# Kernel tuning notes

Hardware: AMD Instinct MI355X
Metric: run time of the kernel (lower is better)

## Reference

```python
import jax, jax.numpy as jnp
import numpy as np

K_TOP = 2  # top-k experts per token (MoE k)


def setup_inputs() -> dict:
    key = jax.random.key(0)
    ks = jax.random.split(key, 4)
    B, D, H, E = 4096, 1024, 2048, 8
    x = jax.random.normal(ks[0], (B, D), dtype=jnp.float32)
    w_gate = jax.random.normal(ks[1], (D, E), dtype=jnp.float32) * 0.02
    W1 = jax.random.normal(ks[2], (E, D, H), dtype=jnp.float32) * (1.0 / np.sqrt(D))
    b1 = jnp.zeros((E, H), dtype=jnp.float32)
    W2 = jax.random.normal(ks[3], (E, H, D), dtype=jnp.float32) * (1.0 / np.sqrt(H))
    b2 = jnp.zeros((E, D), dtype=jnp.float32)
    return {"x": x, "w_gate": w_gate, "W1": W1, "b1": b1, "W2": W2, "b2": b2}


def _top_k_gates(logits, k):
    # noisy_top_k_gating, eval path (noisy_gating=False / train=False):
    # softmax over the top-k logits, scattered back to [B, E]; other gates are 0.
    B, E = logits.shape
    top_logits, top_idx = jax.lax.top_k(logits, k)       # [B, k]
    top_gates = jax.nn.softmax(top_logits, axis=-1)      # [B, k]
    rows = jnp.arange(B)[:, None]
    gates = jnp.zeros((B, E), dtype=logits.dtype).at[rows, top_idx].set(top_gates)
    return gates


def reference(x, w_gate, W1, b1, W2, b2):
    # Gating
    logits = x @ w_gate                                  # [B, E]
    gates = _top_k_gates(logits, K_TOP)                  # [B, E], sparse (top-k nonzero)
    # Experts: MLP(fc1 -> relu -> fc2) per expert. Dense-all-experts form is
    # mathematically identical to dispatch/combine since zero gates contribute 0.
    h = jax.nn.relu(jnp.einsum('bd,edh->beh', x, W1) + b1[None])   # [B, E, H]
    y = jnp.einsum('beh,ehd->bed', h, W2) + b2[None]               # [B, E, D]
    out = jnp.einsum('be,bed->bd', gates, y)                       # gated scatter-combine
    return out
```

## Files before the change

kernel.cpp:

```cpp
#include <hip/hip_runtime.h>

#define B_TOK 4096
#define DDIM  1024
#define HDIM  2048
#define NEXP  8
#define MAXTOK 4096
#define BM 128
#define BN 128
#define BK 64

#define OFF_W1T  0ull
#define OFF_W2T  33554432ull
#define OFF_XB   67108864ull
#define OFF_H    75497472ull
#define OFF_Y    109051904ull
#define OFF_TOK  125829120ull
#define OFF_GATE 125960192ull
#define OFF_PAIR 126091264ull
#define OFF_CNT  126124032ull
#define OFF_OFFS 126124096ull
#define OFF_EIDX (OFF_Y)
#define OFF_GCO  (OFF_Y + 16384ull)

typedef __attribute__((ext_vector_type(4))) float f32x4;
typedef __attribute__((ext_vector_type(8))) short bf16x8;

static __device__ __forceinline__ unsigned short f2bf(float f) {
    unsigned u = __builtin_bit_cast(unsigned, f);
    unsigned r = (u + 0x7FFFu + ((u >> 16) & 1u)) >> 16;
    return (unsigned short)r;
}
static __device__ __forceinline__ float bf2f(unsigned short s) {
    unsigned u = ((unsigned)s) << 16;
    return __builtin_bit_cast(float, u);
}

#define AS1(p) ((const __attribute__((address_space(1))) void*)(p))
#define AS3(p) ((__attribute__((address_space(3))) void*)(p))

__global__ void __launch_bounds__(256) gating_logits_kernel(
    const float* __restrict__ x, const float* __restrict__ wg,
    int* __restrict__ eidx, float* __restrict__ gco, short* __restrict__ Xb) {
    int wave = threadIdx.x >> 6;
    int lane = threadIdx.x & 63;
    int b = blockIdx.x * 4 + wave;
    float acc[NEXP];
#pragma unroll
    for (int e = 0; e < NEXP; e++) acc[e] = 0.f;
    const float* xr = x + (size_t)b * DDIM;
    short* xbr = Xb + (size_t)b * DDIM;
#pragma unroll
    for (int i = 0; i < DDIM / 64; i++) {
        int d = i * 64 + lane;
        float xv = xr[d];
        xbr[d] = (short)f2bf(xv);
        const float4* wrow = (const float4*)(wg + (size_t)d * NEXP);
        float4 w0 = wrow[0], w1 = wrow[1];
        acc[0] += xv * w0.x; acc[1] += xv * w0.y; acc[2] += xv * w0.z; acc[3] += xv * w0.w;
        acc[4] += xv * w1.x; acc[5] += xv * w1.y; acc[6] += xv * w1.z; acc[7] += xv * w1.w;
    }
#pragma unroll
    for (int off = 32; off >= 1; off >>= 1)
#pragma unroll
        for (int e = 0; e < NEXP; e++) acc[e] += __shfl_xor(acc[e], off);
    if (lane == 0) {
        int i1 = 0; float m1 = acc[0];
        for (int e = 1; e < NEXP; e++) if (acc[e] > m1) { m1 = acc[e]; i1 = e; }
        int i2 = (i1 == 0) ? 1 : 0; float m2 = -1e30f;
        for (int e = 0; e < NEXP; e++) { if (e == i1) continue; if (acc[e] > m2) { m2 = acc[e]; i2 = e; } }
        float g1 = 1.f / (1.f + expf(m2 - m1));
        eidx[b] = i1 | (i2 << 16);
        gco[b] = g1;
    }
}

__global__ void __launch_bounds__(256) build_kernel(
    const int* __restrict__ eidx, const float* __restrict__ gco,
    int* __restrict__ counts, int* __restrict__ tok,
    float* __restrict__ gate, int* __restrict__ pair) {
    __shared__ int lhist[NEXP];
    __shared__ int gbase[NEXP];
    int t = threadIdx.x;
    if (t < NEXP) lhist[t] = 0;
    __syncthreads();
    int b = blockIdx.x * 256 + t;
    int ep = eidx[b];
    int e1 = ep & 0xffff, e2 = ep >> 16;
    float g1 = gco[b], g2 = 1.f - g1;
    int l1 = atomicAdd(&lhist[e1], 1);
    int l2 = atomicAdd(&lhist[e2], 1);
    __syncthreads();
    if (t < NEXP) gbase[t] = atomicAdd(&counts[t], lhist[t]);
    __syncthreads();
    int s1 = gbase[e1] + l1, s2 = gbase[e2] + l2;
    tok[e1 * MAXTOK + s1] = b; gate[e1 * MAXTOK + s1] = g1; pair[b * 2 + 0] = e1 * MAXTOK + s1;
    tok[e2 * MAXTOK + s2] = b; gate[e2 * MAXTOK + s2] = g2; pair[b * 2 + 1] = e2 * MAXTOK + s2;
}

__global__ void scan_kernel(const int* __restrict__ counts, int* __restrict__ offs) {
    if (threadIdx.x == 0) {
        int s = 0;
        for (int e = 0; e < NEXP; e++) { offs[e] = s; s += counts[e]; }
    }
}

__global__ void __launch_bounds__(256) tcvt_kernel(const float* __restrict__ src, short* __restrict__ dst,
                                                   int R, int C) {
    __shared__ float tile[64][65];
    int e = blockIdx.z;
    size_t base = (size_t)e * R * C;
    int r0 = blockIdx.y * 64, c0 = blockIdx.x * 64;
    int t = threadIdx.x;
    int rr = t >> 4, c4 = (t & 15) * 4;
    const float* s = src + base + (size_t)r0 * C + c0;
#pragma unroll
    for (int i = 0; i < 4; i++) {
        float4 v = *(const float4*)(s + (size_t)(rr + i * 16) * C + c4);
        tile[rr + i * 16][c4 + 0] = v.x; tile[rr + i * 16][c4 + 1] = v.y;
        tile[rr + i * 16][c4 + 2] = v.z; tile[rr + i * 16][c4 + 3] = v.w;
    }
    __syncthreads();
    short* d = dst + base + (size_t)c0 * R + r0;
    int hr0 = t >> 4, dc = (t & 15) * 4;
#pragma unroll
    for (int i = 0; i < 4; i++) {
        int hr = hr0 + i * 16;
        short4 o;
        o.x = (short)f2bf(tile[dc + 0][hr]); o.y = (short)f2bf(tile[dc + 1][hr]);
        o.z = (short)f2bf(tile[dc + 2][hr]); o.w = (short)f2bf(tile[dc + 3][hr]);
        *(short4*)(d + (size_t)hr * R + dc) = o;
    }
}

__global__ void __launch_bounds__(512, 4) fc1_kernel(
    const short* __restrict__ Xb, const short* __restrict__ W1T, const float* __restrict__ b1,
    short* __restrict__ h, const int* __restrict__ tok,
    const int* __restrict__ counts, const int* __restrict__ offs) {
    int bid = blockIdx.x;
    int e = bid & 7;
    int r2 = bid >> 3;
    int m0 = (r2 & 31) * BM;
    int n0 = (r2 >> 5) * BN;
    int cnt = counts[e];
    if (m0 >= cnt) return;
    int baseh = offs[e];

    __shared__ short As[BM * BK];
    __shared__ short Bs[BN * BK];

    int t = threadIdx.x;
    int wave = t >> 6, lane = t & 63;

    const short* asrc[2]; const short* bsrc[2];
    int dsto[2];
#pragma unroll
    for (int i = 0; i < 2; i++) {
        int G = i * 512 + t;
        int r = G >> 3, q = G & 7;
        int cks = ((q ^ (r & 7)) << 3);
        int trow = m0 + r;
        int tid2 = (trow < cnt) ? tok[e * MAXTOK + trow] : 0;
        asrc[i] = Xb + (size_t)tid2 * DDIM + cks;
        bsrc[i] = W1T + ((size_t)e * HDIM + n0 + r) * DDIM + cks;
        dsto[i] = G * 8;
    }

    int wr = wave >> 2, wc = wave & 3;
    f32x4 acc[4][2];
    f32x4 zero = {0.f, 0.f, 0.f, 0.f};
#pragma unroll
    for (int m = 0; m < 4; m++)
#pragma unroll
        for (int n = 0; n < 2; n++) acc[m][n] = zero;

    int l15 = lane & 15, l7 = lane & 7, lhi = lane >> 4;
    int aoff[4][2], boff[2][2];
#pragma unroll
    for (int ks = 0; ks < 2; ks++) {
        int q = (lhi + ks * 4) ^ l7;
#pragma unroll
        for (int m = 0; m < 4; m++) aoff[m][ks] = (wr * 64 + m * 16 + l15) * BK + (q << 3);
#pragma unroll
        for (int n = 0; n < 2; n++) boff[n][ks] = (wc * 32 + n * 16 + l15) * BK + (q << 3);
    }

    const int NT = DDIM / BK;
    for (int kt = 0; kt < NT; ++kt) {
        int k0 = kt * BK;
#pragma unroll
        for (int i = 0; i < 2; i++) {
            __builtin_amdgcn_global_load_lds(AS1(asrc[i] + k0), AS3(&As[dsto[i]]), 16, 0, 0);
            __builtin_amdgcn_global_load_lds(AS1(bsrc[i] + k0), AS3(&Bs[dsto[i]]), 16, 0, 0);
        }
        __syncthreads();
        bf16x8 af[4][2], bg[2][2];
#pragma unroll
        for (int ks = 0; ks < 2; ks++) {
#pragma unroll
            for (int m = 0; m < 4; m++) af[m][ks] = *(const bf16x8*)(&As[aoff[m][ks]]);
#pragma unroll
            for (int n = 0; n < 2; n++) bg[n][ks] = *(const bf16x8*)(&Bs[boff[n][ks]]);
        }
        __builtin_amdgcn_s_setprio(1);
#pragma unroll
        for (int ks = 0; ks < 2; ks++)
#pragma unroll
            for (int m = 0; m < 4; m++)
#pragma unroll
                for (int n = 0; n < 2; n++)
                    acc[m][n] = __builtin_amdgcn_mfma_f32_16x16x32_bf16(bg[n][ks], af[m][ks], acc[m][n], 0, 0, 0);
        __builtin_amdgcn_s_setprio(0);
        __syncthreads();
    }

#pragma unroll
    for (int m = 0; m < 4; m++) {
        int row = m0 + wr * 64 + m * 16 + l15;
        if (row < cnt) {
            size_t rb = (size_t)(baseh + row) * HDIM;
#pragma unroll
            for (int n = 0; n < 2; n++) {
                int colb = n0 + wc * 32 + n * 16 + (lhi << 2);
                float4 bias = *(const float4*)(b1 + e * HDIM + colb);
                float v0 = acc[m][n][0] + bias.x; v0 = v0 > 0.f ? v0 : 0.f;
                float v1 = acc[m][n][1] + bias.y; v1 = v1 > 0.f ? v1 : 0.f;
                float v2 = acc[m][n][2] + bias.z; v2 = v2 > 0.f ? v2 : 0.f;
                float v3 = acc[m][n][3] + bias.w; v3 = v3 > 0.f ? v3 : 0.f;
                short4 o;
                o.x = (short)f2bf(v0); o.y = (short)f2bf(v1);
                o.z = (short)f2bf(v2); o.w = (short)f2bf(v3);
                *(short4*)(h + rb + colb) = o;
            }
        }
    }
}

__global__ void __launch_bounds__(512, 4) fc2_kernel(
    const short* __restrict__ h, const short* __restrict__ W2T, const float* __restrict__ b2,
    short* __restrict__ ybuf, const int* __restrict__ counts, const int* __restrict__ offs) {
    int bid = blockIdx.x;
    int e = bid & 7;
    int r2 = bid >> 3;
    int m0 = (r2 & 31) * BM;
    int n0 = (r2 >> 5) * BN;
    int cnt = counts[e];
    if (m0 >= cnt) return;
    int baseh = offs[e];

    __shared__ short As[BM * BK];
    __shared__ short Bs[BN * BK];

    int t = threadIdx.x;
    int wave = t >> 6, lane = t & 63;

    const short* asrc[2]; const short* bsrc[2];
    int dsto[2];
#pragma unroll
    for (int i = 0; i < 2; i++) {
        int G = i * 512 + t;
        int r = G >> 3, q = G & 7;
        int cks = ((q ^ (r & 7)) << 3);
        asrc[i] = h + (size_t)(baseh + m0 + r) * HDIM + cks;
        bsrc[i] = W2T + ((size_t)e * DDIM + n0 + r) * HDIM + cks;
        dsto[i] = G * 8;
    }

    int wr = wave >> 2, wc = wave & 3;
    f32x4 acc[4][2];
    f32x4 zero = {0.f, 0.f, 0.f, 0.f};
#pragma unroll
    for (int m = 0; m < 4; m++)
#pragma unroll
        for (int n = 0; n < 2; n++) acc[m][n] = zero;

    int l15 = lane & 15, l7 = lane & 7, lhi = lane >> 4;
    int aoff[4][2], boff[2][2];
#pragma unroll
    for (int ks = 0; ks < 2; ks++) {
        int q = (lhi + ks * 4) ^ l7;
#pragma unroll
        for (int m = 0; m < 4; m++) aoff[m][ks] = (wr * 64 + m * 16 + l15) * BK + (q << 3);
#pragma unroll
        for (int n = 0; n < 2; n++) boff[n][ks] = (wc * 32 + n * 16 + l15) * BK + (q << 3);
    }

    const int NT = HDIM / BK;
    for (int kt = 0; kt < NT; ++kt) {
        int k0 = kt * BK;
#pragma unroll
        for (int i = 0; i < 2; i++) {
            __builtin_amdgcn_global_load_lds(AS1(asrc[i] + k0), AS3(&As[dsto[i]]), 16, 0, 0);
            __builtin_amdgcn_global_load_lds(AS1(bsrc[i] + k0), AS3(&Bs[dsto[i]]), 16, 0, 0);
        }
        __syncthreads();
        bf16x8 af[4][2], bg[2][2];
#pragma unroll
        for (int ks = 0; ks < 2; ks++) {
#pragma unroll
            for (int m = 0; m < 4; m++) af[m][ks] = *(const bf16x8*)(&As[aoff[m][ks]]);
#pragma unroll
            for (int n = 0; n < 2; n++) bg[n][ks] = *(const bf16x8*)(&Bs[boff[n][ks]]);
        }
        __builtin_amdgcn_s_setprio(1);
#pragma unroll
        for (int ks = 0; ks < 2; ks++)
#pragma unroll
            for (int m = 0; m < 4; m++)
#pragma unroll
                for (int n = 0; n < 2; n++)
                    acc[m][n] = __builtin_amdgcn_mfma_f32_16x16x32_bf16(bg[n][ks], af[m][ks], acc[m][n], 0, 0, 0);
        __builtin_amdgcn_s_setprio(0);
        __syncthreads();
    }

#pragma unroll
    for (int m = 0; m < 4; m++) {
        int row = m0 + wr * 64 + m * 16 + l15;
        if (row < cnt) {
            size_t rb = (size_t)(baseh + row) * DDIM;
#pragma unroll
            for (int n = 0; n < 2; n++) {
                int colb = n0 + wc * 32 + n * 16 + (lhi << 2);
                float4 bias = *(const float4*)(b2 + e * DDIM + colb);
                short4 o;
                o.x = (short)f2bf(acc[m][n][0] + bias.x);
                o.y = (short)f2bf(acc[m][n][1] + bias.y);
                o.z = (short)f2bf(acc[m][n][2] + bias.z);
                o.w = (short)f2bf(acc[m][n][3] + bias.w);
                *(short4*)(ybuf + rb + colb) = o;
            }
        }
    }
}

__global__ void __launch_bounds__(256) combine_kernel(
    const short* __restrict__ ybuf, const float* __restrict__ gate,
    const int* __restrict__ pair, const int* __restrict__ offs, float* __restrict__ out) {
    int b = blockIdx.x;
    int p0 = pair[b * 2], p1 = pair[b * 2 + 1];
    float g0 = gate[p0], g1 = gate[p1];
    int r0 = offs[p0 >> 12] + (p0 & 4095);
    int r1 = offs[p1 >> 12] + (p1 & 4095);
    const short4* y0 = (const short4*)(ybuf + (size_t)r0 * DDIM);
    const short4* y1 = (const short4*)(ybuf + (size_t)r1 * DDIM);
    float4* o = (float4*)(out + (size_t)b * DDIM);
    int t = threadIdx.x;
    short4 a = y0[t], c = y1[t];
    float4 v;
    v.x = g0 * bf2f((unsigned short)a.x) + g1 * bf2f((unsigned short)c.x);
    v.y = g0 * bf2f((unsigned short)a.y) + g1 * bf2f((unsigned short)c.y);
    v.z = g0 * bf2f((unsigned short)a.z) + g1 * bf2f((unsigned short)c.z);
    v.w = g0 * bf2f((unsigned short)a.w) + g1 * bf2f((unsigned short)c.w);
    o[t] = v;
}

extern "C" void kernel_launch(void* const* d_in, const int* in_sizes, int n_in,
                              void* d_out, int out_size, void* d_ws, size_t ws_size,
                              hipStream_t stream) {
    const float* x  = (const float*)d_in[0];
    const float* wg = (const float*)d_in[1];
    const float* W1 = (const float*)d_in[2];
    const float* b1 = (const float*)d_in[3];
    const float* W2 = (const float*)d_in[4];
    const float* b2 = (const float*)d_in[5];
    float* out = (float*)d_out;
    char* ws = (char*)d_ws;

    short* W1T = (short*)(ws + OFF_W1T);
    short* W2T = (short*)(ws + OFF_W2T);
    short* Xb  = (short*)(ws + OFF_XB);
    short* h   = (short*)(ws + OFF_H);
    short* ybuf = (short*)(ws + OFF_Y);
    int* tok   = (int*)(ws + OFF_TOK);
    float* gate = (float*)(ws + OFF_GATE);
    int* pair  = (int*)(ws + OFF_PAIR);
    int* counts = (int*)(ws + OFF_CNT);
    int* offs  = (int*)(ws + OFF_OFFS);
    int* eidx  = (int*)(ws + OFF_EIDX);
    float* gco = (float*)(ws + OFF_GCO);

    hipMemsetAsync(counts, 0, 64, stream);
    gating_logits_kernel<<<B_TOK / 4, 256, 0, stream>>>(x, wg, eidx, gco, Xb);
    build_kernel<<<B_TOK / 256, 256, 0, stream>>>(eidx, gco, counts, tok, gate, pair);
    scan_kernel<<<1, 64, 0, stream>>>(counts, offs);
    tcvt_kernel<<<dim3(HDIM / 64, DDIM / 64, NEXP), 256, 0, stream>>>(W1, W1T, DDIM, HDIM);
    tcvt_kernel<<<dim3(DDIM / 64, HDIM / 64, NEXP), 256, 0, stream>>>(W2, W2T, HDIM, DDIM);
    fc1_kernel<<<NEXP * 32 * (HDIM / BN), 512, 0, stream>>>(Xb, W1T, b1, h, tok, counts, offs);
    fc2_kernel<<<NEXP * 32 * (DDIM / BN), 512, 0, stream>>>(h, W2T, b2, ybuf, counts, offs);
    combine_kernel<<<B_TOK, 256, 0, stream>>>(ybuf, gate, pair, offs, out);
}
```

Before: 197.0 us.

## Use 4-wave blocks with 64x64 per-wave tiles in expert GEMMs

Both expert GEMM kernels switch from 8 waves per 128x128 tile, each computing 64x32, to 4 waves each computing a 64x64 sub-tile with a 4x4 MFMA accumulator grid. Each thread now issues twice as many global-to-LDS loads, and fragment loads are interleaved per k-step. The aim is more MFMA work per LDS fragment read, giving better register-level reuse and fewer waves contending for LDS. The cost is higher register pressure and fewer waves per CU for hiding latency, with launch bounds lowered to 256 threads and a minimum of 3 blocks.

```diff
diff --git a/kernel.cpp b/kernel.cpp
--- a/kernel.cpp
+++ b/kernel.cpp
@@ -132,7 +132,7 @@
     }
 }
 
-__global__ void __launch_bounds__(512, 4) fc1_kernel(
+__global__ void __launch_bounds__(256, 3) fc1_kernel(
     const short* __restrict__ Xb, const short* __restrict__ W1T, const float* __restrict__ b1,
     short* __restrict__ h, const int* __restrict__ tok,
     const int* __restrict__ counts, const int* __restrict__ offs) {
@@ -151,11 +151,11 @@
     int t = threadIdx.x;
     int wave = t >> 6, lane = t & 63;
 
-    const short* asrc[2]; const short* bsrc[2];
-    int dsto[2];
-#pragma unroll
-    for (int i = 0; i < 2; i++) {
-        int G = i * 512 + t;
+    const short* asrc[4]; const short* bsrc[4];
+    int dsto[4];
+#pragma unroll
+    for (int i = 0; i < 4; i++) {
+        int G = i * 256 + t;
         int r = G >> 3, q = G & 7;
         int cks = ((q ^ (r & 7)) << 3);
         int trow = m0 + r;
@@ -165,62 +165,62 @@
         dsto[i] = G * 8;
     }
 
-    int wr = wave >> 2, wc = wave & 3;
-    f32x4 acc[4][2];
+    int wr = (wave >> 1) * 64, wc = (wave & 1) * 64;
+    f32x4 acc[4][4];
     f32x4 zero = {0.f, 0.f, 0.f, 0.f};
 #pragma unroll
     for (int m = 0; m < 4; m++)
 #pragma unroll
-        for (int n = 0; n < 2; n++) acc[m][n] = zero;
+        for (int n = 0; n < 4; n++) acc[m][n] = zero;
 
     int l15 = lane & 15, l7 = lane & 7, lhi = lane >> 4;
-    int aoff[4][2], boff[2][2];
+    int aoff[4][2], boff[4][2];
 #pragma unroll
     for (int ks = 0; ks < 2; ks++) {
         int q = (lhi + ks * 4) ^ l7;
 #pragma unroll
-        for (int m = 0; m < 4; m++) aoff[m][ks] = (wr * 64 + m * 16 + l15) * BK + (q << 3);
-#pragma unroll
-        for (int n = 0; n < 2; n++) boff[n][ks] = (wc * 32 + n * 16 + l15) * BK + (q << 3);
+        for (int m = 0; m < 4; m++) {
+            aoff[m][ks] = (wr + m * 16 + l15) * BK + (q << 3);
+            boff[m][ks] = (wc + m * 16 + l15) * BK + (q << 3);
+        }
     }
 
     const int NT = DDIM / BK;
     for (int kt = 0; kt < NT; ++kt) {
         int k0 = kt * BK;
 #pragma unroll
-        for (int i = 0; i < 2; i++) {
+        for (int i = 0; i < 4; i++) {
             __builtin_amdgcn_global_load_lds(AS1(asrc[i] + k0), AS3(&As[dsto[i]]), 16, 0, 0);
             __builtin_amdgcn_global_load_lds(AS1(bsrc[i] + k0), AS3(&Bs[dsto[i]]), 16, 0, 0);
         }
         __syncthreads();
-        bf16x8 af[4][2], bg[2][2];
 #pragma unroll
         for (int ks = 0; ks < 2; ks++) {
-#pragma unroll
-            for (int m = 0; m < 4; m++) af[m][ks] = *(const bf16x8*)(&As[aoff[m][ks]]);
-#pragma unroll
-            for (int n = 0; n < 2; n++) bg[n][ks] = *(const bf16x8*)(&Bs[boff[n][ks]]);
-        }
-        __builtin_amdgcn_s_setprio(1);
-#pragma unroll
-        for (int ks = 0; ks < 2; ks++)
+            bf16x8 af[4], bg[4];
+#pragma unroll
+            for (int m = 0; m < 4; m++) {
+                af[m] = *(const bf16x8*)(&As[aoff[m][ks]]);
+                bg[m] = *(const bf16x8*)(&Bs[boff[m][ks]]);
+            }
+            __builtin_amdgcn_s_setprio(1);
 #pragma unroll
             for (int m = 0; m < 4; m++)
 #pragma unroll
-                for (int n = 0; n < 2; n++)
-                    acc[m][n] = __builtin_amdgcn_mfma_f32_16x16x32_bf16(bg[n][ks], af[m][ks], acc[m][n], 0, 0, 0);
-        __builtin_amdgcn_s_setprio(0);
+                for (int n = 0; n < 4; n++)
+                    acc[m][n] = __builtin_amdgcn_mfma_f32_16x16x32_bf16(bg[n], af[m], acc[m][n], 0, 0, 0);
+            __builtin_amdgcn_s_setprio(0);
+        }
         __syncthreads();
     }
 
 #pragma unroll
     for (int m = 0; m < 4; m++) {
-        int row = m0 + wr * 64 + m * 16 + l15;
+        int row = m0 + wr + m * 16 + l15;
         if (row < cnt) {
             size_t rb = (size_t)(baseh + row) * HDIM;
 #pragma unroll
-            for (int n = 0; n < 2; n++) {
-                int colb = n0 + wc * 32 + n * 16 + (lhi << 2);
+            for (int n = 0; n < 4; n++) {
+                int colb = n0 + wc + n * 16 + (lhi << 2);
                 float4 bias = *(const float4*)(b1 + e * HDIM + colb);
                 float v0 = acc[m][n][0] + bias.x; v0 = v0 > 0.f ? v0 : 0.f;
                 float v1 = acc[m][n][1] + bias.y; v1 = v1 > 0.f ? v1 : 0.f;
@@ -235,7 +235,7 @@
     }
 }
 
-__global__ void __launch_bounds__(512, 4) fc2_kernel(
+__global__ void __launch_bounds__(256, 3) fc2_kernel(
     const short* __restrict__ h, const short* __restrict__ W2T, const float* __restrict__ b2,
     short* __restrict__ ybuf, const int* __restrict__ counts, const int* __restrict__ offs) {
     int bid = blockIdx.x;
@@ -253,11 +253,11 @@
     int t = threadIdx.x;
     int wave = t >> 6, lane = t & 63;
 
-    const short* asrc[2]; const short* bsrc[2];
-    int dsto[2];
-#pragma unroll
-    for (int i = 0; i < 2; i++) {
-        int G = i * 512 + t;
+    const short* asrc[4]; const short* bsrc[4];
+    int dsto[4];
+#pragma unroll
+    for (int i = 0; i < 4; i++) {
+        int G = i * 256 + t;
         int r = G >> 3, q = G & 7;
         int cks = ((q ^ (r & 7)) << 3);
         asrc[i] = h + (size_t)(baseh + m0 + r) * HDIM + cks;
@@ -265,62 +265,62 @@
         dsto[i] = G * 8;
     }
 
-    int wr = wave >> 2, wc = wave & 3;
-    f32x4 acc[4][2];
+    int wr = (wave >> 1) * 64, wc = (wave & 1) * 64;
+    f32x4 acc[4][4];
     f32x4 zero = {0.f, 0.f, 0.f, 0.f};
 #pragma unroll
     for (int m = 0; m < 4; m++)
 #pragma unroll
-        for (int n = 0; n < 2; n++) acc[m][n] = zero;
+        for (int n = 0; n < 4; n++) acc[m][n] = zero;
 
     int l15 = lane & 15, l7 = lane & 7, lhi = lane >> 4;
-    int aoff[4][2], boff[2][2];
+    int aoff[4][2], boff[4][2];
 #pragma unroll
     for (int ks = 0; ks < 2; ks++) {
         int q = (lhi + ks * 4) ^ l7;
 #pragma unroll
-        for (int m = 0; m < 4; m++) aoff[m][ks] = (wr * 64 + m * 16 + l15) * BK + (q << 3);
-#pragma unroll
-        for (int n = 0; n < 2; n++) boff[n][ks] = (wc * 32 + n * 16 + l15) * BK + (q << 3);
+        for (int m = 0; m < 4; m++) {
+            aoff[m][ks] = (wr + m * 16 + l15) * BK + (q << 3);
+            boff[m][ks] = (wc + m * 16 + l15) * BK + (q << 3);
+        }
     }
 
     const int NT = HDIM / BK;
     for (int kt = 0; kt < NT; ++kt) {
         int k0 = kt * BK;
 #pragma unroll
-        for (int i = 0; i < 2; i++) {
+        for (int i = 0; i < 4; i++) {
             __builtin_amdgcn_global_load_lds(AS1(asrc[i] + k0), AS3(&As[dsto[i]]), 16, 0, 0);
             __builtin_amdgcn_global_load_lds(AS1(bsrc[i] + k0), AS3(&Bs[dsto[i]]), 16, 0, 0);
         }
         __syncthreads();
-        bf16x8 af[4][2], bg[2][2];
 #pragma unroll
         for (int ks = 0; ks < 2; ks++) {
-#pragma unroll
-            for (int m = 0; m < 4; m++) af[m][ks] = *(const bf16x8*)(&As[aoff[m][ks]]);
-#pragma unroll
-            for (int n = 0; n < 2; n++) bg[n][ks] = *(const bf16x8*)(&Bs[boff[n][ks]]);
-        }
-        __builtin_amdgcn_s_setprio(1);
-#pragma unroll
-        for (int ks = 0; ks < 2; ks++)
+            bf16x8 af[4], bg[4];
+#pragma unroll
+            for (int m = 0; m < 4; m++) {
+                af[m] = *(const bf16x8*)(&As[aoff[m][ks]]);
+                bg[m] = *(const bf16x8*)(&Bs[boff[m][ks]]);
+            }
+            __builtin_amdgcn_s_setprio(1);
 #pragma unroll
             for (int m = 0; m < 4; m++)
 #pragma unroll
-                for (int n = 0; n < 2; n++)
-                    acc[m][n] = __builtin_amdgcn_mfma_f32_16x16x32_bf16(bg[n][ks], af[m][ks], acc[m][n], 0, 0, 0);
-        __builtin_amdgcn_s_setprio(0);
+                for (int n = 0; n < 4; n++)
+                    acc[m][n] = __builtin_amdgcn_mfma_f32_16x16x32_bf16(bg[n], af[m], acc[m][n], 0, 0, 0);
+            __builtin_amdgcn_s_setprio(0);
+        }
         __syncthreads();
     }
 
 #pragma unroll
     for (int m = 0; m < 4; m++) {
-        int row = m0 + wr * 64 + m * 16 + l15;
+        int row = m0 + wr + m * 16 + l15;
         if (row < cnt) {
             size_t rb = (size_t)(baseh + row) * DDIM;
 #pragma unroll
-            for (int n = 0; n < 2; n++) {
-                int colb = n0 + wc * 32 + n * 16 + (lhi << 2);
+            for (int n = 0; n < 4; n++) {
+                int colb = n0 + wc + n * 16 + (lhi << 2);
                 float4 bias = *(const float4*)(b2 + e * DDIM + colb);
                 short4 o;
                 o.x = (short)f2bf(acc[m][n][0] + bias.x);
@@ -385,7 +385,7 @@
     scan_kernel<<<1, 64, 0, stream>>>(counts, offs);
     tcvt_kernel<<<dim3(HDIM / 64, DDIM / 64, NEXP), 256, 0, stream>>>(W1, W1T, DDIM, HDIM);
     tcvt_kernel<<<dim3(DDIM / 64, HDIM / 64, NEXP), 256, 0, stream>>>(W2, W2T, HDIM, DDIM);
-    fc1_kernel<<<NEXP * 32 * (HDIM / BN), 512, 0, stream>>>(Xb, W1T, b1, h, tok, counts, offs);
-    fc2_kernel<<<NEXP * 32 * (DDIM / BN), 512, 0, stream>>>(h, W2T, b2, ybuf, counts, offs);
+    fc1_kernel<<<NEXP * 32 * (HDIM / BN), 256, 0, stream>>>(Xb, W1T, b1, h, tok, counts, offs);
+    fc2_kernel<<<NEXP * 32 * (DDIM / BN), 256, 0, stream>>>(h, W2T, b2, ybuf, counts, offs);
     combine_kernel<<<B_TOK, 256, 0, stream>>>(ybuf, gate, pair, offs, out);
 }
```

After: 187.4 us. 4.9% less time.
